# Performance work log

Measured on AMD Instinct MI355X. Metric: run time of the kernel, lower is better.

Reference implementation:

```python
import jax, jax.numpy as jnp
import numpy as np

B, S, H = 2, 2048, 1024
NH = 16
HD = H // NH

def setup_inputs() -> dict:
    key = jax.random.key(0)
    ks = jax.random.split(key, 9)
    s = 1.0 / np.sqrt(H)
    return {
        "hidden_state": jax.random.normal(ks[0], (B, S, H), dtype=jnp.float32),
        "Wq": jax.random.normal(ks[1], (H, H), dtype=jnp.float32) * s,
        "bq": jnp.zeros((H,), dtype=jnp.float32),
        "Wk": jax.random.normal(ks[2], (H, H), dtype=jnp.float32) * s,
        "bk": jnp.zeros((H,), dtype=jnp.float32),
        "Wv": jax.random.normal(ks[3], (H, H), dtype=jnp.float32) * s,
        "bv": jnp.zeros((H,), dtype=jnp.float32),
        "Wo": jax.random.normal(ks[4], (H, H), dtype=jnp.float32) * s,
        "bo": jnp.zeros((H,), dtype=jnp.float32),
    }

def reference(hidden_state, Wq, bq, Wk, bk, Wv, bv, Wo, bo):
    x = hidden_state  # [B,S,H]
    def split(t):
        return t.reshape(B, S, NH, HD).transpose(0, 2, 1, 3)  # [B,NH,S,HD]
    q = split(x @ Wq.T + bq)
    k = split(x @ Wk.T + bk)
    v = split(x @ Wv.T + bv)
    scale = 1.0 / jnp.sqrt(jnp.asarray(HD, dtype=x.dtype))
    scores = jnp.einsum('bhqd,bhkd->bhqk', q, k) * scale  # [B,NH,S,S]
    probs = jax.nn.softmax(scores, axis=-1)
    out = jnp.einsum('bhqk,bhkd->bhqd', probs, v)  # [B,NH,S,HD]
    out = out.transpose(0, 2, 1, 3).reshape(B, S, H)
    return out @ Wo.T + bo
```

## Files before the change

### kernel.cpp

```cpp
#include <hip/hip_runtime.h>


#define BD 2
#define SD 2048
#define HDIM 1024
#define NHD 16
#define HDD 64
#define NTOK 4096
#define QSCALE 0.1803368801111204f

typedef float f32x4 __attribute__((ext_vector_type(4)));
typedef _Float16 f16x8 __attribute__((ext_vector_type(8)));
typedef _Float16 f16x4 __attribute__((ext_vector_type(4)));

__device__ __forceinline__ f32x4 mfma_f16(f16x8 a, f16x8 b, f32x4 c) {
  return __builtin_amdgcn_mfma_f32_16x16x32_f16(a, b, c, 0, 0, 0);
}

__global__ void convert_kernel(const float* __restrict__ x,
                               const float* __restrict__ wq, const float* __restrict__ wk,
                               const float* __restrict__ wv, const float* __restrict__ wo,
                               _Float16* __restrict__ dst) {
  const int total4 = (8 * 1024 * 1024) / 4;
  for (int idx = blockIdx.x * blockDim.x + threadIdx.x; idx < total4;
       idx += gridDim.x * blockDim.x) {
    int e = idx * 4;
    const float* s;
    if (e < 4 * 1024 * 1024) {
      s = x + e;
    } else {
      int w = (e - 4 * 1024 * 1024) >> 20;
      int off = e & 1048575;
      s = (w == 0 ? wq : w == 1 ? wk : w == 2 ? wv : wo) + off;
    }
    float4 v = *(const float4*)s;
    f16x4 h;
    h[0] = (_Float16)v.x; h[1] = (_Float16)v.y;
    h[2] = (_Float16)v.z; h[3] = (_Float16)v.w;
    *(f16x4*)(dst + e) = h;
  }
}

__device__ __forceinline__ void gemm_mainloop(
    const _Float16* __restrict__ Ap, const _Float16* __restrict__ Bp,
    int i0, int j0, _Float16* As, _Float16* Bs, f32x4 acc[4][4]) {
  const int tid = threadIdx.x;
  const int wid = tid >> 6, lane = tid & 63;
  const int lr = lane & 15, lg = lane >> 4;
  const int wm = wid >> 1, wn = wid & 1;
  const int srow = lane >> 2;
  const int scol = (lane & 3) * 8;

  for (int k0 = 0; k0 < HDIM; k0 += 32) {
#pragma unroll
    for (int it = 0; it < 2; ++it) {
      int rb = (wid * 2 + it) * 16;
      const _Float16* ga = Ap + (size_t)(i0 + rb + srow) * HDIM + k0 + scol;
      const _Float16* gb = Bp + (size_t)(j0 + rb + srow) * HDIM + k0 + scol;
      __builtin_amdgcn_global_load_lds(
          (__attribute__((address_space(1))) void*)ga,
          (__attribute__((address_space(3))) void*)(As + (wid * 2 + it) * 512), 16, 0, 0);
      __builtin_amdgcn_global_load_lds(
          (__attribute__((address_space(1))) void*)gb,
          (__attribute__((address_space(3))) void*)(Bs + (wid * 2 + it) * 512), 16, 0, 0);
    }
    __syncthreads();
    f16x8 af[4], bf[4];
#pragma unroll
    for (int mt = 0; mt < 4; mt++)
      af[mt] = *(const f16x8*)(As + (wm * 64 + mt * 16 + lr) * 32 + lg * 8);
#pragma unroll
    for (int nt = 0; nt < 4; nt++)
      bf[nt] = *(const f16x8*)(Bs + (wn * 64 + nt * 16 + lr) * 32 + lg * 8);
#pragma unroll
    for (int mt = 0; mt < 4; mt++)
#pragma unroll
      for (int nt = 0; nt < 4; nt++)
        acc[mt][nt] = mfma_f16(af[mt], bf[nt], acc[mt][nt]);
    __syncthreads();
  }
}

__global__ __launch_bounds__(256) void gemm_qkv(
    const _Float16* __restrict__ xb,
    const _Float16* __restrict__ wqb, const _Float16* __restrict__ wkb,
    const _Float16* __restrict__ wvb,
    const float* __restrict__ bq, const float* __restrict__ bk,
    const float* __restrict__ bv,
    _Float16* __restrict__ Qo, _Float16* __restrict__ Ko, _Float16* __restrict__ Vt) {
  __shared__ __attribute__((aligned(16))) _Float16 As[128 * 32];
  __shared__ __attribute__((aligned(16))) _Float16 Bs[128 * 32];
  const int bx = blockIdx.x;
  const int mat = bx >> 8;
  const int sub = bx & 255;
  const _Float16 *Ap, *Bp;
  int i0, j0;
  if (mat < 2) {
    Ap = xb; Bp = (mat ? wkb : wqb);
    i0 = (sub >> 3) * 128;
    j0 = (sub & 7) * 128;
  } else {
    Ap = wvb; Bp = xb;
    i0 = (sub & 7) * 128;
    j0 = (sub >> 3) * 128;
  }
  f32x4 acc[4][4];
#pragma unroll
  for (int a = 0; a < 4; a++)
#pragma unroll
    for (int b = 0; b < 4; b++) acc[a][b] = (f32x4){0.f, 0.f, 0.f, 0.f};

  gemm_mainloop(Ap, Bp, i0, j0, As, Bs, acc);

  const int tid = threadIdx.x;
  const int wid = tid >> 6, lane = tid & 63;
  const int lr = lane & 15, lg = lane >> 4;
  const int wm = wid >> 1, wn = wid & 1;
  const float* bias = (mat == 0 ? bq : mat == 1 ? bk : bv);

#pragma unroll
  for (int mt = 0; mt < 4; mt++) {
#pragma unroll
    for (int nt = 0; nt < 4; nt++) {
      int i = i0 + wm * 64 + mt * 16 + 4 * lg;
      int j = j0 + wn * 64 + nt * 16 + lr;
      if (mat < 2) {
        float bj = bias[j];
        int h = j >> 6, d = j & 63;
        _Float16* dst = (mat ? Ko : Qo);
        float scl = (mat == 0) ? QSCALE : 1.0f;
#pragma unroll
        for (int r = 0; r < 4; r++) {
          int tok = i + r;
          int b = tok >> 11, s = tok & 2047;
          dst[(((size_t)(b * NHD + h)) * SD + s) * HDD + d] =
              (_Float16)((acc[mt][nt][r] + bj) * scl);
        }
      } else {
        int tok = j;
        int b = tok >> 11, s = tok & 2047;
#pragma unroll
        for (int r = 0; r < 4; r++) {
          int wr = i + r;
          int h = wr >> 6, d = wr & 63;
          Vt[((size_t)(b * NHD + h) * HDD + d) * SD + s] =
              (_Float16)(acc[mt][nt][r] + bias[wr]);
        }
      }
    }
  }
}

__global__ __launch_bounds__(256) void gemm_out(
    const _Float16* __restrict__ attn, const _Float16* __restrict__ wob,
    const float* __restrict__ bo, float* __restrict__ out) {
  __shared__ __attribute__((aligned(16))) _Float16 As[128 * 32];
  __shared__ __attribute__((aligned(16))) _Float16 Bs[128 * 32];
  const int sub = blockIdx.x;
  const int i0 = (sub >> 3) * 128, j0 = (sub & 7) * 128;
  f32x4 acc[4][4];
#pragma unroll
  for (int a = 0; a < 4; a++)
#pragma unroll
    for (int b = 0; b < 4; b++) acc[a][b] = (f32x4){0.f, 0.f, 0.f, 0.f};

  gemm_mainloop(attn, wob, i0, j0, As, Bs, acc);

  const int tid = threadIdx.x;
  const int wid = tid >> 6, lane = tid & 63;
  const int lr = lane & 15, lg = lane >> 4;
  const int wm = wid >> 1, wn = wid & 1;
#pragma unroll
  for (int mt = 0; mt < 4; mt++) {
#pragma unroll
    for (int nt = 0; nt < 4; nt++) {
      int i = i0 + wm * 64 + mt * 16 + 4 * lg;
      int j = j0 + wn * 64 + nt * 16 + lr;
      float bj = bo[j];
#pragma unroll
      for (int r = 0; r < 4; r++)
        out[(size_t)(i + r) * HDIM + j] = acc[mt][nt][r] + bj;
    }
  }
}

__global__ __launch_bounds__(256) void attn_kernel(
    const _Float16* __restrict__ Q, const _Float16* __restrict__ K,
    const _Float16* __restrict__ VT, _Float16* __restrict__ AO) {
  const int bh = blockIdx.y, qb = blockIdx.x;
  const int tid = threadIdx.x, wv = tid >> 6, lane = tid & 63;
  const int lr = lane & 15, lg = lane >> 4;
  const int q0 = qb * 64 + wv * 16;
  const _Float16* Qh = Q + (size_t)bh * SD * HDD;
  const _Float16* Kh = K + (size_t)bh * SD * HDD;
  const _Float16* Vh = VT + (size_t)bh * HDD * SD;

  __shared__ __attribute__((aligned(16))) _Float16 Ks[2][2][64][32];
  __shared__ __attribute__((aligned(16))) _Float16 Vs[2][2][64][32];

  const int krow = lane >> 2;
  const int kswz = (((lane & 3) ^ ((lane >> 3) & 3)) * 8);

  const int m  = lane & 15;
  const int u  = m & 3;
  const int sg = m >> 2;
  const int r4 = lane >> 4;
  const int c2 = (r4 >> 1) & 1;
  const int keyoff_e = 16 * (u >> 1) + 4 * (sg ^ c2)       + 2 * (u & 1);
  const int keyoff_o = 16 * (u >> 1) + 4 * (sg ^ (c2 | 2)) + 2 * (u & 1);
  const _Float16* Vrow[4];
#pragma unroll
  for (int i = 0; i < 4; i++)
    Vrow[i] = Vh + (size_t)(wv * 16 + i * 4 + r4) * SD + ((i & 1) ? keyoff_o : keyoff_e);

  auto stage = [&](int b, int kv0) {
#pragma unroll
    for (int kf = 0; kf < 2; kf++) {
      const _Float16* gk = Kh + (size_t)(kv0 + wv * 16 + krow) * HDD + kf * 32 + kswz;
      __builtin_amdgcn_global_load_lds(
          (__attribute__((address_space(1))) void*)gk,
          (__attribute__((address_space(3))) void*)(&Ks[b][kf][wv * 16][0]), 16, 0, 0);
    }
#pragma unroll
    for (int kf = 0; kf < 2; kf++)
#pragma unroll
      for (int i = 0; i < 4; i++) {
        const _Float16* gv = Vrow[i] + kv0 + kf * 32;
        __builtin_amdgcn_global_load_lds(
            (__attribute__((address_space(1))) void*)gv,
            (__attribute__((address_space(3))) void*)(&Vs[b][kf][wv * 16 + i * 4][0]), 4, 0, 0);
      }
  };

  const int fswz = (lg ^ ((lr >> 1) & 3)) * 8;

  f16x8 qf[2];
#pragma unroll
  for (int kf = 0; kf < 2; kf++)
    qf[kf] = *(const f16x8*)(Qh + (size_t)(q0 + lr) * HDD + kf * 32 + lg * 8);

  f32x4 acc[4];
#pragma unroll
  for (int i = 0; i < 4; i++) acc[i] = (f32x4){0.f, 0.f, 0.f, 0.f};
  float mrun = -1e30f, lsum = 0.f;

  stage(0, 0);
  int cur = 0;

  for (int t = 0; t < SD / 64; ++t) {
    asm volatile("s_waitcnt vmcnt(0)" ::: "memory");
    __builtin_amdgcn_s_barrier();
    stage(cur ^ 1, ((t + 1) & (SD / 64 - 1)) * 64);

    f32x4 sc[4];
#pragma unroll
    for (int nt = 0; nt < 4; nt++) sc[nt] = (f32x4){0.f, 0.f, 0.f, 0.f};
#pragma unroll
    for (int nt = 0; nt < 4; nt++)
#pragma unroll
      for (int kf = 0; kf < 2; kf++) {
        f16x8 kfr = *(const f16x8*)&Ks[cur][kf][nt * 16 + lr][fswz];
        sc[nt] = mfma_f16(kfr, qf[kf], sc[nt]);
      }

    float tm = sc[0][0];
#pragma unroll
    for (int nt = 0; nt < 4; nt++)
#pragma unroll
      for (int r = 0; r < 4; r++) tm = fmaxf(tm, sc[nt][r]);
    tm = fmaxf(tm, __shfl_xor(tm, 16));
    tm = fmaxf(tm, __shfl_xor(tm, 32));

    if (__any(tm - mrun > 8.0f)) {
      float mn = fmaxf(mrun, tm);
      float fm = exp2f(mrun - mn);
      mrun = mn;
      lsum *= fm;
#pragma unroll
      for (int ntd = 0; ntd < 4; ntd++)
#pragma unroll
        for (int r = 0; r < 4; r++) acc[ntd][r] *= fm;
    }

    float p[4][4];
#pragma unroll
    for (int nt = 0; nt < 4; nt++)
#pragma unroll
      for (int r = 0; r < 4; r++) {
        p[nt][r] = exp2f(sc[nt][r] - mrun);
        lsum += p[nt][r];
      }

#pragma unroll
    for (int kf = 0; kf < 2; kf++) {
      f16x8 pb;
#pragma unroll
      for (int r = 0; r < 4; r++) {
        pb[r]     = (_Float16)p[2 * kf][r];
        pb[4 + r] = (_Float16)p[2 * kf + 1][r];
      }
#pragma unroll
      for (int ntd = 0; ntd < 4; ntd++) {
        f16x8 vf = *(const f16x8*)&Vs[cur][kf][ntd * 16 + lr][fswz];
        acc[ntd] = mfma_f16(vf, pb, acc[ntd]);
      }
    }
    cur ^= 1;
  }

  lsum += __shfl_xor(lsum, 16);
  lsum += __shfl_xor(lsum, 32);
  float inv = 1.0f / lsum;

  const int b = bh >> 4, h = bh & 15;
  _Float16* aoRow = AO + (size_t)(b * SD + q0 + lr) * HDIM + h * 64;
#pragma unroll
  for (int ntd = 0; ntd < 4; ntd++) {
    f16x4 o;
#pragma unroll
    for (int r = 0; r < 4; r++) o[r] = (_Float16)(acc[ntd][r] * inv);
    *(f16x4*)(aoRow + ntd * 16 + 4 * lg) = o;
  }
}

extern "C" void kernel_launch(void* const* d_in, const int* in_sizes, int n_in,
                              void* d_out, int out_size, void* d_ws, size_t ws_size,
                              hipStream_t stream) {
  const float* x  = (const float*)d_in[0];
  const float* Wq = (const float*)d_in[1];
  const float* bq = (const float*)d_in[2];
  const float* Wk = (const float*)d_in[3];
  const float* bk = (const float*)d_in[4];
  const float* Wv = (const float*)d_in[5];
  const float* bv = (const float*)d_in[6];
  const float* Wo = (const float*)d_in[7];
  const float* bo = (const float*)d_in[8];
  float* out = (float*)d_out;

  _Float16* xb  = (_Float16*)d_ws;
  _Float16* wqb = xb + 4 * 1024 * 1024;
  _Float16* wkb = wqb + 1024 * 1024;
  _Float16* wvb = wkb + 1024 * 1024;
  _Float16* wob = wvb + 1024 * 1024;
  _Float16* Qb  = wob + 1024 * 1024;
  _Float16* Kb  = Qb + 4 * 1024 * 1024;
  _Float16* Vt  = Kb + 4 * 1024 * 1024;
  _Float16* AOb = Vt + 4 * 1024 * 1024;

  convert_kernel<<<dim3(1024), dim3(256), 0, stream>>>(x, Wq, Wk, Wv, Wo, xb);
  gemm_qkv<<<dim3(768), dim3(256), 0, stream>>>(xb, wqb, wkb, wvb, bq, bk, bv, Qb, Kb, Vt);
  attn_kernel<<<dim3(32, 32), dim3(256), 0, stream>>>(Qb, Kb, Vt, AOb);
  gemm_out<<<dim3(256), dim3(256), 0, stream>>>(AOb, wob, bo, out);
}
```

Measured before the change: 155.5 us.

## Restructure attention: 32 queries per wave, triple-buffered KV, XCD-aware grid, pre-permuted V

Each attention wave now handles two 16-row query tiles, so every K/V fragment read from LDS feeds twice the MFMA work. The grid is halved to 512 blocks and remapped so the heads placed on one XCD share K/V in L2. Staging moves to a three-deep LDS ring with partial vmcnt waits, so loads run further ahead of compute. The QKV GEMM now writes V^T with keys permuted inside each 64-key block, which lets V be staged with 16-byte loads instead of 4-byte ones. It also adds packed RTZ f16 conversion for P and s_setprio around the MFMA sections, at the cost of more registers and LDS, which may reduce occupancy.

```diff
diff --git a/kernel.cpp b/kernel.cpp
--- a/kernel.cpp
+++ b/kernel.cpp
@@ -12,9 +12,15 @@
 typedef float f32x4 __attribute__((ext_vector_type(4)));
 typedef _Float16 f16x8 __attribute__((ext_vector_type(8)));
 typedef _Float16 f16x4 __attribute__((ext_vector_type(4)));
+typedef __fp16 fp16x2 __attribute__((ext_vector_type(2)));
 
 __device__ __forceinline__ f32x4 mfma_f16(f16x8 a, f16x8 b, f32x4 c) {
   return __builtin_amdgcn_mfma_f32_16x16x32_f16(a, b, c, 0, 0, 0);
+}
+
+__device__ __forceinline__ unsigned int pk2h(float lo, float hi) {
+  fp16x2 v = __builtin_amdgcn_cvt_pkrtz(lo, hi);
+  return __builtin_bit_cast(unsigned int, v);
 }
 
 __global__ void convert_kernel(const float* __restrict__ x,
@@ -139,11 +145,14 @@
       } else {
         int tok = j;
         int b = tok >> 11, s = tok & 2047;
+        int w = s & 63;
+        int pos = (w & 32) + ((w & 12) << 1) + ((w & 16) >> 2) + (w & 3);
+        int sp = (s & ~63) | pos;
 #pragma unroll
         for (int r = 0; r < 4; r++) {
           int wr = i + r;
           int h = wr >> 6, d = wr & 63;
-          Vt[((size_t)(b * NHD + h) * HDD + d) * SD + s] =
+          Vt[((size_t)(b * NHD + h) * HDD + d) * SD + sp] =
               (_Float16)(acc[mt][nt][r] + bias[wr]);
         }
       }
@@ -187,139 +196,173 @@
 __global__ __launch_bounds__(256) void attn_kernel(
     const _Float16* __restrict__ Q, const _Float16* __restrict__ K,
     const _Float16* __restrict__ VT, _Float16* __restrict__ AO) {
-  const int bh = blockIdx.y, qb = blockIdx.x;
+  const int g = blockIdx.x;
+  const int xcd = g & 7, idx = g >> 3;
+  const int qb = idx & 15;
+  const int bh = xcd * 4 + (idx >> 4);
   const int tid = threadIdx.x, wv = tid >> 6, lane = tid & 63;
   const int lr = lane & 15, lg = lane >> 4;
-  const int q0 = qb * 64 + wv * 16;
+  const int q0 = qb * 128 + wv * 32;
   const _Float16* Qh = Q + (size_t)bh * SD * HDD;
   const _Float16* Kh = K + (size_t)bh * SD * HDD;
   const _Float16* Vh = VT + (size_t)bh * HDD * SD;
 
-  __shared__ __attribute__((aligned(16))) _Float16 Ks[2][2][64][32];
-  __shared__ __attribute__((aligned(16))) _Float16 Vs[2][2][64][32];
+  __shared__ __attribute__((aligned(16))) _Float16 Ks[3][2][64][32];
+  __shared__ __attribute__((aligned(16))) _Float16 Vs[3][2][64][32];
 
   const int krow = lane >> 2;
   const int kswz = (((lane & 3) ^ ((lane >> 3) & 3)) * 8);
-
-  const int m  = lane & 15;
-  const int u  = m & 3;
-  const int sg = m >> 2;
-  const int r4 = lane >> 4;
-  const int c2 = (r4 >> 1) & 1;
-  const int keyoff_e = 16 * (u >> 1) + 4 * (sg ^ c2)       + 2 * (u & 1);
-  const int keyoff_o = 16 * (u >> 1) + 4 * (sg ^ (c2 | 2)) + 2 * (u & 1);
-  const _Float16* Vrow[4];
-#pragma unroll
-  for (int i = 0; i < 4; i++)
-    Vrow[i] = Vh + (size_t)(wv * 16 + i * 4 + r4) * SD + ((i & 1) ? keyoff_o : keyoff_e);
+  const int kkf = wv & 1, krb = (wv >> 1) * 32;
 
   auto stage = [&](int b, int kv0) {
 #pragma unroll
-    for (int kf = 0; kf < 2; kf++) {
-      const _Float16* gk = Kh + (size_t)(kv0 + wv * 16 + krow) * HDD + kf * 32 + kswz;
+    for (int i = 0; i < 2; ++i) {
+      const _Float16* gk =
+          Kh + (size_t)(kv0 + krb + i * 16 + krow) * HDD + kkf * 32 + kswz;
       __builtin_amdgcn_global_load_lds(
           (__attribute__((address_space(1))) void*)gk,
-          (__attribute__((address_space(3))) void*)(&Ks[b][kf][wv * 16][0]), 16, 0, 0);
-    }
-#pragma unroll
-    for (int kf = 0; kf < 2; kf++)
-#pragma unroll
-      for (int i = 0; i < 4; i++) {
-        const _Float16* gv = Vrow[i] + kv0 + kf * 32;
-        __builtin_amdgcn_global_load_lds(
-            (__attribute__((address_space(1))) void*)gv,
-            (__attribute__((address_space(3))) void*)(&Vs[b][kf][wv * 16 + i * 4][0]), 4, 0, 0);
-      }
+          (__attribute__((address_space(3))) void*)(&Ks[b][kkf][krb + i * 16][0]), 16, 0, 0);
+      const _Float16* gv =
+          Vh + (size_t)(krb + i * 16 + krow) * SD + kv0 + kkf * 32 + kswz;
+      __builtin_amdgcn_global_load_lds(
+          (__attribute__((address_space(1))) void*)gv,
+          (__attribute__((address_space(3))) void*)(&Vs[b][kkf][krb + i * 16][0]), 16, 0, 0);
+    }
   };
 
   const int fswz = (lg ^ ((lr >> 1) & 3)) * 8;
 
-  f16x8 qf[2];
-#pragma unroll
-  for (int kf = 0; kf < 2; kf++)
-    qf[kf] = *(const f16x8*)(Qh + (size_t)(q0 + lr) * HDD + kf * 32 + lg * 8);
-
-  f32x4 acc[4];
-#pragma unroll
-  for (int i = 0; i < 4; i++) acc[i] = (f32x4){0.f, 0.f, 0.f, 0.f};
-  float mrun = -1e30f, lsum = 0.f;
+  f16x8 qfA[2], qfB[2];
+#pragma unroll
+  for (int kf = 0; kf < 2; kf++) {
+    qfA[kf] = *(const f16x8*)(Qh + (size_t)(q0 + lr) * HDD + kf * 32 + lg * 8);
+    qfB[kf] = *(const f16x8*)(Qh + (size_t)(q0 + 16 + lr) * HDD + kf * 32 + lg * 8);
+  }
+
+  f32x4 accA[4], accB[4];
+#pragma unroll
+  for (int i = 0; i < 4; i++) {
+    accA[i] = (f32x4){0.f, 0.f, 0.f, 0.f};
+    accB[i] = (f32x4){0.f, 0.f, 0.f, 0.f};
+  }
+  float mrunA = -1e30f, mrunB = -1e30f;
+  float lsA0 = 0.f, lsA1 = 0.f, lsB0 = 0.f, lsB1 = 0.f;
 
   stage(0, 0);
+  stage(1, 64);
   int cur = 0;
 
   for (int t = 0; t < SD / 64; ++t) {
-    asm volatile("s_waitcnt vmcnt(0)" ::: "memory");
+    asm volatile("s_waitcnt vmcnt(4)" ::: "memory");
     __builtin_amdgcn_s_barrier();
-    stage(cur ^ 1, ((t + 1) & (SD / 64 - 1)) * 64);
-
-    f32x4 sc[4];
-#pragma unroll
-    for (int nt = 0; nt < 4; nt++) sc[nt] = (f32x4){0.f, 0.f, 0.f, 0.f};
+    int nb = cur + 2; if (nb >= 3) nb -= 3;
+    stage(nb, ((t + 2) & (SD / 64 - 1)) * 64);
+
+    f32x4 scA[4], scB[4];
+#pragma unroll
+    for (int nt = 0; nt < 4; nt++) {
+      scA[nt] = (f32x4){0.f, 0.f, 0.f, 0.f};
+      scB[nt] = (f32x4){0.f, 0.f, 0.f, 0.f};
+    }
+    __builtin_amdgcn_s_setprio(1);
 #pragma unroll
     for (int nt = 0; nt < 4; nt++)
 #pragma unroll
       for (int kf = 0; kf < 2; kf++) {
         f16x8 kfr = *(const f16x8*)&Ks[cur][kf][nt * 16 + lr][fswz];
-        sc[nt] = mfma_f16(kfr, qf[kf], sc[nt]);
+        scA[nt] = mfma_f16(kfr, qfA[kf], scA[nt]);
+        scB[nt] = mfma_f16(kfr, qfB[kf], scB[nt]);
       }
-
-    float tm = sc[0][0];
-#pragma unroll
-    for (int nt = 0; nt < 4; nt++)
-#pragma unroll
-      for (int r = 0; r < 4; r++) tm = fmaxf(tm, sc[nt][r]);
-    tm = fmaxf(tm, __shfl_xor(tm, 16));
-    tm = fmaxf(tm, __shfl_xor(tm, 32));
-
-    if (__any(tm - mrun > 8.0f)) {
-      float mn = fmaxf(mrun, tm);
-      float fm = exp2f(mrun - mn);
-      mrun = mn;
-      lsum *= fm;
+    __builtin_amdgcn_s_setprio(0);
+
+    float a0 = fmaxf(fmaxf(scA[0][0], scA[0][1]), scA[0][2]);
+    float a1 = fmaxf(fmaxf(scA[0][3], scA[1][0]), scA[1][1]);
+    float a2 = fmaxf(fmaxf(scA[1][2], scA[1][3]), scA[2][0]);
+    float a3 = fmaxf(fmaxf(scA[2][1], scA[2][2]), scA[2][3]);
+    float a4 = fmaxf(fmaxf(scA[3][0], scA[3][1]), scA[3][2]);
+    float tmA = fmaxf(fmaxf(fmaxf(a0, a1), fmaxf(a2, a3)), fmaxf(a4, scA[3][3]));
+    float b0 = fmaxf(fmaxf(scB[0][0], scB[0][1]), scB[0][2]);
+    float b1 = fmaxf(fmaxf(scB[0][3], scB[1][0]), scB[1][1]);
+    float b2 = fmaxf(fmaxf(scB[1][2], scB[1][3]), scB[2][0]);
+    float b3 = fmaxf(fmaxf(scB[2][1], scB[2][2]), scB[2][3]);
+    float b4 = fmaxf(fmaxf(scB[3][0], scB[3][1]), scB[3][2]);
+    float tmB = fmaxf(fmaxf(fmaxf(b0, b1), fmaxf(b2, b3)), fmaxf(b4, scB[3][3]));
+    tmA = fmaxf(tmA, __shfl_xor(tmA, 16));
+    tmA = fmaxf(tmA, __shfl_xor(tmA, 32));
+    tmB = fmaxf(tmB, __shfl_xor(tmB, 16));
+    tmB = fmaxf(tmB, __shfl_xor(tmB, 32));
+
+    if (__any(fmaxf(tmA - mrunA, tmB - mrunB) > 8.0f)) {
+      float mnA = fmaxf(mrunA, tmA);
+      float fmA = exp2f(mrunA - mnA);
+      mrunA = mnA; lsA0 *= fmA; lsA1 *= fmA;
+      float mnB = fmaxf(mrunB, tmB);
+      float fmB = exp2f(mrunB - mnB);
+      mrunB = mnB; lsB0 *= fmB; lsB1 *= fmB;
 #pragma unroll
       for (int ntd = 0; ntd < 4; ntd++)
 #pragma unroll
-        for (int r = 0; r < 4; r++) acc[ntd][r] *= fm;
-    }
-
-    float p[4][4];
-#pragma unroll
-    for (int nt = 0; nt < 4; nt++)
-#pragma unroll
-      for (int r = 0; r < 4; r++) {
-        p[nt][r] = exp2f(sc[nt][r] - mrun);
-        lsum += p[nt][r];
-      }
+        for (int r = 0; r < 4; r++) {
+          accA[ntd][r] *= fmA;
+          accB[ntd][r] *= fmB;
+        }
+    }
 
 #pragma unroll
     for (int kf = 0; kf < 2; kf++) {
-      f16x8 pb;
-#pragma unroll
-      for (int r = 0; r < 4; r++) {
-        pb[r]     = (_Float16)p[2 * kf][r];
-        pb[4 + r] = (_Float16)p[2 * kf + 1][r];
-      }
+      float pa0[4], pa1[4], pb0[4], pb1[4];
+#pragma unroll
+      for (int r = 0; r < 4; r++) pa0[r] = exp2f(scA[2 * kf][r] - mrunA);
+#pragma unroll
+      for (int r = 0; r < 4; r++) pa1[r] = exp2f(scA[2 * kf + 1][r] - mrunA);
+#pragma unroll
+      for (int r = 0; r < 4; r++) pb0[r] = exp2f(scB[2 * kf][r] - mrunB);
+#pragma unroll
+      for (int r = 0; r < 4; r++) pb1[r] = exp2f(scB[2 * kf + 1][r] - mrunB);
+      lsA0 += (pa0[0] + pa0[1]) + (pa0[2] + pa0[3]);
+      lsA1 += (pa1[0] + pa1[1]) + (pa1[2] + pa1[3]);
+      lsB0 += (pb0[0] + pb0[1]) + (pb0[2] + pb0[3]);
+      lsB1 += (pb1[0] + pb1[1]) + (pb1[2] + pb1[3]);
+      unsigned int wA[4], wB[4];
+      wA[0] = pk2h(pa0[0], pa0[1]); wA[1] = pk2h(pa0[2], pa0[3]);
+      wA[2] = pk2h(pa1[0], pa1[1]); wA[3] = pk2h(pa1[2], pa1[3]);
+      wB[0] = pk2h(pb0[0], pb0[1]); wB[1] = pk2h(pb0[2], pb0[3]);
+      wB[2] = pk2h(pb1[0], pb1[1]); wB[3] = pk2h(pb1[2], pb1[3]);
+      f16x8 pbA = __builtin_bit_cast(f16x8, *(unsigned int(*)[4])wA);
+      f16x8 pbB = __builtin_bit_cast(f16x8, *(unsigned int(*)[4])wB);
+      __builtin_amdgcn_s_setprio(1);
 #pragma unroll
       for (int ntd = 0; ntd < 4; ntd++) {
         f16x8 vf = *(const f16x8*)&Vs[cur][kf][ntd * 16 + lr][fswz];
-        acc[ntd] = mfma_f16(vf, pb, acc[ntd]);
+        accA[ntd] = mfma_f16(vf, pbA, accA[ntd]);
+        accB[ntd] = mfma_f16(vf, pbB, accB[ntd]);
       }
-    }
-    cur ^= 1;
-  }
-
-  lsum += __shfl_xor(lsum, 16);
-  lsum += __shfl_xor(lsum, 32);
-  float inv = 1.0f / lsum;
+      __builtin_amdgcn_s_setprio(0);
+    }
+    cur = (cur + 1 == 3) ? 0 : cur + 1;
+  }
+
+  float lsumA = lsA0 + lsA1;
+  float lsumB = lsB0 + lsB1;
+  lsumA += __shfl_xor(lsumA, 16);
+  lsumA += __shfl_xor(lsumA, 32);
+  lsumB += __shfl_xor(lsumB, 16);
+  lsumB += __shfl_xor(lsumB, 32);
+  float invA = 1.0f / lsumA, invB = 1.0f / lsumB;
 
   const int b = bh >> 4, h = bh & 15;
-  _Float16* aoRow = AO + (size_t)(b * SD + q0 + lr) * HDIM + h * 64;
+  _Float16* aoA = AO + (size_t)(b * SD + q0 + lr) * HDIM + h * 64;
+  _Float16* aoB = AO + (size_t)(b * SD + q0 + 16 + lr) * HDIM + h * 64;
 #pragma unroll
   for (int ntd = 0; ntd < 4; ntd++) {
-    f16x4 o;
-#pragma unroll
-    for (int r = 0; r < 4; r++) o[r] = (_Float16)(acc[ntd][r] * inv);
-    *(f16x4*)(aoRow + ntd * 16 + 4 * lg) = o;
+    f16x4 oA, oB;
+#pragma unroll
+    for (int r = 0; r < 4; r++) {
+      oA[r] = (_Float16)(accA[ntd][r] * invA);
+      oB[r] = (_Float16)(accB[ntd][r] * invB);
+    }
+    *(f16x4*)(aoA + ntd * 16 + 4 * lg) = oA;
+    *(f16x4*)(aoB + ntd * 16 + 4 * lg) = oB;
   }
 }
 
@@ -349,6 +392,6 @@
 
   convert_kernel<<<dim3(1024), dim3(256), 0, stream>>>(x, Wq, Wk, Wv, Wo, xb);
   gemm_qkv<<<dim3(768), dim3(256), 0, stream>>>(xb, wqb, wkb, wvb, bq, bk, bv, Qb, Kb, Vt);
-  attn_kernel<<<dim3(32, 32), dim3(256), 0, stream>>>(Qb, Kb, Vt, AOb);
+  attn_kernel<<<dim3(512), dim3(256), 0, stream>>>(Qb, Kb, Vt, AOb);
   gemm_out<<<dim3(256), dim3(256), 0, stream>>>(AOb, wob, bo, out);
 }
```

Measured after the change: 146.8 us. 1.06x faster.
